# Performance work log

Measured on AMD Instinct MI355X. Metric: run time of the kernel, lower is better.

## Reference

```python
import jax, jax.numpy as jnp
import numpy as np

# BoxCoder weights and clamp from the torch module
WX, WY, WW, WH = 10.0, 10.0, 5.0, 5.0
BBOX_CLIP = float(np.log(1000.0 / 16.0))
SCORE_THRESH = 0.05
NMS_THRESH = 0.5
DET_PER_IMG = 100
MIN_SIZE = 0.01
B, N, C = 4, 4096, 91
IMG_H, IMG_W = 800, 1216


def setup_inputs() -> dict:
    key = jax.random.key(0)
    k1, k2, k3, k4, k5, k6 = jax.random.split(key, 6)
    class_logits = jax.random.normal(k1, (B * N, C), dtype=jnp.float32) * 2.0
    box_regression = jax.random.normal(k2, (B * N, C * 4), dtype=jnp.float32) * 0.5
    # valid xyxy proposals inside the image
    x1 = jax.random.uniform(k3, (B, N)) * (0.7 * IMG_W)
    y1 = jax.random.uniform(k4, (B, N)) * (0.7 * IMG_H)
    bw = jax.random.uniform(k5, (B, N)) * (0.25 * IMG_W) + 4.0
    bh = jax.random.uniform(k6, (B, N)) * (0.25 * IMG_H) + 4.0
    proposals = jnp.stack([x1, y1, x1 + bw, y1 + bh], axis=-1)
    image_shapes = jnp.tile(jnp.array([[IMG_H, IMG_W]], dtype=jnp.int32), (B, 1))
    return {"class_logits": class_logits, "box_regression": box_regression,
            "proposals": proposals, "image_shapes": image_shapes}


def decode_boxes(deltas, proposals):
    # deltas [N, C, 4], proposals [N, 4] xyxy -> pred boxes [N, C, 4]
    w = proposals[:, 2] - proposals[:, 0]
    h = proposals[:, 3] - proposals[:, 1]
    cx = proposals[:, 0] + 0.5 * w
    cy = proposals[:, 1] + 0.5 * h
    dx = deltas[..., 0] / WX
    dy = deltas[..., 1] / WY
    dw = jnp.minimum(deltas[..., 2] / WW, BBOX_CLIP)
    dh = jnp.minimum(deltas[..., 3] / WH, BBOX_CLIP)
    pcx = dx * w[:, None] + cx[:, None]
    pcy = dy * h[:, None] + cy[:, None]
    pw = jnp.exp(dw) * w[:, None]
    ph = jnp.exp(dh) * h[:, None]
    return jnp.stack([pcx - 0.5 * pw, pcy - 0.5 * ph,
                      pcx + 0.5 * pw, pcy + 0.5 * ph], axis=-1)


def iou_one_many(box, boxes):
    # box [4] vs boxes [M, 4]
    lt = jnp.maximum(box[:2], boxes[:, :2])
    rb = jnp.minimum(box[2:], boxes[:, 2:])
    wh = jnp.clip(rb - lt, 0.0)
    inter = wh[:, 0] * wh[:, 1]
    a1 = (box[2] - box[0]) * (box[3] - box[1])
    a2 = (boxes[:, 2] - boxes[:, 0]) * (boxes[:, 3] - boxes[:, 1])
    return inter / (a1 + a2 - inter)


def nms_keep(off_boxes, live):
    # greedy NMS on class-offset boxes; selection is non-differentiable
    off_boxes = jax.lax.stop_gradient(off_boxes)
    live = jax.lax.stop_gradient(live)

    def body(lv, _):
        i = jnp.argmax(lv)
        s = lv[i]
        iou = iou_one_many(off_boxes[i], off_boxes)
        lv = jnp.where(iou > NMS_THRESH, -jnp.inf, lv)
        lv = lv.at[i].set(-jnp.inf)
        return lv, (i, jnp.isfinite(s))

    _, (keep, kvalid) = jax.lax.scan(body, live, None, length=DET_PER_IMG)
    return keep, kvalid  # [DET_PER_IMG] each


def postprocess_one(logits, deltas, proposals, hw):
    # logits [N, C], deltas [N, C*4], proposals [N, 4], hw [2] float (H, W)
    num_classes = logits.shape[-1]
    boxes = decode_boxes(deltas.reshape(-1, num_classes, 4), proposals)  # [N, C, 4]
    Hh, Ww = hw[0], hw[1]
    boxes = jnp.stack([jnp.clip(boxes[..., 0], 0.0, Ww),
                       jnp.clip(boxes[..., 1], 0.0, Hh),
                       jnp.clip(boxes[..., 2], 0.0, Ww),
                       jnp.clip(boxes[..., 3], 0.0, Hh)], axis=-1)
    scores = jax.nn.softmax(logits, axis=-1)
    labels = jnp.broadcast_to(jnp.arange(num_classes, dtype=jnp.int32), scores.shape)
    # drop background class 0, flatten per-class candidates -> M = N*(C-1)
    boxes = boxes[:, 1:].reshape(-1, 4)
    scores = scores[:, 1:].reshape(-1)
    labels = labels[:, 1:].reshape(-1)
    ws = boxes[:, 2] - boxes[:, 0]
    hs = boxes[:, 3] - boxes[:, 1]
    valid = (scores > SCORE_THRESH) & (ws >= MIN_SIZE) & (hs >= MIN_SIZE)
    # batched_nms: per-class coordinate offset so classes never overlap
    max_coord = jnp.max(boxes)
    off_boxes = boxes + (labels.astype(boxes.dtype) * (max_coord + 1.0))[:, None]
    live = jnp.where(valid, scores, -jnp.inf)
    keep, kvalid = nms_keep(off_boxes, live)
    out_boxes = jnp.where(kvalid[:, None], boxes[keep], 0.0)
    out_scores = jnp.where(kvalid, scores[keep], 0.0)
    out_labels = jnp.where(kvalid, labels[keep], -1)
    return out_boxes, out_scores, out_labels


def reference(class_logits, box_regression, proposals, image_shapes):
    b, n, _ = proposals.shape
    num_classes = class_logits.shape[-1]
    logits = class_logits.reshape(b, n, num_classes)
    deltas = box_regression.reshape(b, n, num_classes * 4)
    hw = image_shapes.astype(logits.dtype)
    boxes, scores, labels = jax.vmap(postprocess_one)(logits, deltas, proposals, hw)
    return boxes, scores, labels
```

## Files before the change

kernel.cpp:

```cpp
#include <hip/hip_runtime.h>
#include <math.h>
#include <float.h>
#include <limits.h>

#define NBATCH 4
#define NPROP  4096
#define NCLS   91
#define NFG    90
#define NDET   100
#define CCAP   1024
#define BN     (NBATCH * NPROP)
#define SLOTS  (NFG * NDET)
#define FCAP   16384
#define CHUNK  128

static __device__ __forceinline__ float clampf(float x, float lo, float hi) {
    return fminf(fmaxf(x, lo), hi);
}

static __device__ __forceinline__ void decode_box(int b, int np, int c,
    const float* __restrict__ props, const float* __restrict__ deltas,
    float W, float H, float& bx1, float& by1, float& bx2, float& by2)
{
    const float* pr = props + ((size_t)b * NPROP + np) * 4;
    const float x1 = pr[0], y1 = pr[1], x2 = pr[2], y2 = pr[3];
    const float w = x2 - x1, h = y2 - y1;
    const float cx = x1 + 0.5f * w, cy = y1 + 0.5f * h;
    const float* d = deltas + (((size_t)b * NPROP + np) * NCLS + c) * 4;
    const float BBC = 4.135166556742356f;
    const float dx = d[0] / 10.0f;
    const float dy = d[1] / 10.0f;
    const float dw = fminf(d[2] / 5.0f, BBC);
    const float dh = fminf(d[3] / 5.0f, BBC);
    const float pcx = dx * w + cx;
    const float pcy = dy * h + cy;
    const float pw = expf(dw) * w;
    const float ph = expf(dh) * h;
    bx1 = clampf(pcx - 0.5f * pw, 0.0f, W);
    by1 = clampf(pcy - 0.5f * ph, 0.0f, H);
    bx2 = clampf(pcx + 0.5f * pw, 0.0f, W);
    by2 = clampf(pcy + 0.5f * ph, 0.0f, H);
}

static __device__ __forceinline__ bool iou_gt(const float4 S, const float4 Q, float aq)
{
    const float iw = fmaxf(fminf(S.z, Q.z) - fmaxf(S.x, Q.x), 0.0f);
    const float ih = fmaxf(fminf(S.w, Q.w) - fmaxf(S.y, Q.y), 0.0f);
    const float inter = iw * ih;
    const float as = (S.z - S.x) * (S.w - S.y);
    return inter / (as + aq - inter) > 0.5f;
}

static __device__ __forceinline__ int block_excl_scan(int v, int t, int* wtot)
{
    const int lane = t & 63, wid = t >> 6;
    int inc = v;
    #pragma unroll
    for (int s = 1; s < 64; s <<= 1) {
        const int u = __shfl_up(inc, s);
        if (lane >= s) inc += u;
    }
    if (lane == 63) wtot[wid] = inc;
    __syncthreads();
    int base = 0;
    for (int w2 = 0; w2 < wid; ++w2) base += wtot[w2];
    __syncthreads();
    return base + inc - v;
}

__global__ __launch_bounds__(256) void stats_mask_kernel(
    const float* __restrict__ logits, const float* __restrict__ props,
    const float* __restrict__ deltas, const int* __restrict__ imgsh,
    float2* __restrict__ stats, unsigned* __restrict__ mask)
{
    const int wavei = threadIdx.x >> 6;
    const int lane  = threadIdx.x & 63;
    const int p = blockIdx.x * 4 + wavei;
    const int b = p >> 12;
    const int np = p & (NPROP - 1);
    const float* lrow = logits + (size_t)p * NCLS;

    const float a  = lrow[lane];
    const float a2 = (lane + 64 < NCLS) ? lrow[lane + 64] : -INFINITY;

    float m = fmaxf(a, a2);
    #pragma unroll
    for (int s = 32; s > 0; s >>= 1) m = fmaxf(m, __shfl_down(m, s));
    m = __shfl(m, 0);

    const float e0 = expf(a - m);
    const float e1 = (lane + 64 < NCLS) ? expf(a2 - m) : 0.0f;
    float sum = e0 + e1;
    #pragma unroll
    for (int s = 32; s > 0; s >>= 1) sum += __shfl_down(sum, s);
    sum = __shfl(sum, 0);

    const float W = (float)imgsh[b * 2 + 1];
    const float H = (float)imgsh[b * 2 + 0];

    bool pass0 = ((e0 / sum) > 0.05f) && (lane >= 1);
    if (pass0) {
        float bx1, by1, bx2, by2;
        decode_box(b, np, lane, props, deltas, W, H, bx1, by1, bx2, by2);
        pass0 = ((bx2 - bx1) >= 0.01f) && ((by2 - by1) >= 0.01f);
    }
    bool pass1 = ((e1 / sum) > 0.05f);
    if (pass1) {
        float bx1, by1, bx2, by2;
        decode_box(b, np, lane + 64, props, deltas, W, H, bx1, by1, bx2, by2);
        pass1 = ((bx2 - bx1) >= 0.01f) && ((by2 - by1) >= 0.01f);
    }

    const unsigned long long b0 = __ballot(pass0);
    const unsigned long long b1 = __ballot(pass1);

    if (lane == 0) {
        stats[p] = make_float2(m, sum);
        mask[p]          = (unsigned)b0;
        mask[BN + p]     = (unsigned)(b0 >> 32);
        mask[2 * BN + p] = (unsigned)b1;
    }
}

__global__ __launch_bounds__(256) void class_nms_kernel(
    const float* __restrict__ logits, const float2* __restrict__ stats,
    const unsigned* __restrict__ mask,
    const float* __restrict__ props, const float* __restrict__ deltas,
    const int* __restrict__ imgsh, unsigned long long* __restrict__ svKeys)
{
    const int blk  = blockIdx.x;
    const int b    = blk / NFG;
    const int cm1  = blk % NFG;
    const int c    = cm1 + 1;
    const int t    = threadIdx.x;
    const int lane = t & 63;
    const int wid  = t >> 6;

    __shared__ unsigned long long sk[CCAP];
    __shared__ unsigned long long sks[CCAP];
    __shared__ float4 sbox[CCAP];
    __shared__ unsigned long long mrow[CHUNK][2];
    __shared__ float4 sOwn[NDET];
    __shared__ unsigned long long sPreW[2];
    __shared__ int wtot[4];
    __shared__ int s_ns;

    const float W = (float)imgsh[b * 2 + 1];
    const float H = (float)imgsh[b * 2 + 0];

    const unsigned* mp = mask + (size_t)(c >> 5) * BN + b * NPROP;
    const unsigned bit = 1u << (c & 31);

    int cnt = 0;
    #pragma unroll 4
    for (int np = t; np < NPROP; np += 256) cnt += (mp[np] & bit) ? 1 : 0;

    int v = cnt;
    #pragma unroll
    for (int s = 1; s < 64; s <<= 1) {
        const int u = __shfl_up(v, s);
        if (lane >= s) v += u;
    }
    if (lane == 63) wtot[wid] = v;
    __syncthreads();
    int base = 0;
    for (int w2 = 0; w2 < wid; ++w2) base += wtot[w2];
    int pos = base + v - cnt;
    const int ntot = wtot[0] + wtot[1] + wtot[2] + wtot[3];
    const int n = min(ntot, CCAP);
    if (n == 0) {
        for (int i = t; i < NDET; i += 256) svKeys[(size_t)blk * NDET + i] = 0ULL;
        return;
    }

    for (int np = t; np < NPROP; np += 256) {
        if (!(mp[np] & bit)) continue;
        const int p = b * NPROP + np;
        const float lg = logits[(size_t)p * NCLS + c];
        const float2 st = stats[p];
        const float score = expf(lg - st.x) / st.y;
        const unsigned flat = (unsigned)(np * NFG + cm1);
        const unsigned long long key =
            ((unsigned long long)__float_as_uint(score) << 32) | (unsigned)(~flat);
        if (pos < CCAP) sk[pos] = key;
        ++pos;
    }
    __syncthreads();

    {
        unsigned long long myk[4];
        int rnk[4] = {0, 0, 0, 0};
        #pragma unroll
        for (int e = 0; e < 4; ++e)
            myk[e] = (t + e * 256 < n) ? sk[t + e * 256] : 0ULL;
        #pragma unroll 4
        for (int j = 0; j < n; ++j) {
            const unsigned long long kj = sk[j];
            #pragma unroll
            for (int e = 0; e < 4; ++e) rnk[e] += (kj > myk[e]) ? 1 : 0;
        }
        #pragma unroll
        for (int e = 0; e < 4; ++e)
            if (t + e * 256 < n) sks[rnk[e]] = myk[e];
    }
    __syncthreads();

    for (int i = t; i < n; i += 256) {
        const unsigned flat = ~(unsigned)sks[i];
        const int np = flat / NFG;
        float bx1, by1, bx2, by2;
        decode_box(b, np, c, props, deltas, W, H, bx1, by1, bx2, by2);
        sbox[i] = make_float4(bx1, by1, bx2, by2);
    }
    if (t == 0) s_ns = 0;
    __syncthreads();

    int nsTot = 0;
    for (int cb = 0; cb < n && nsTot < NDET; cb += CHUNK) {
        const int C = min(CHUNK, n - cb);

        bool pre = false;
        if (t < C) {
            const float4 Q = sbox[cb + t];
            const float aq = (Q.z - Q.x) * (Q.w - Q.y);
            for (int l = 0; l < nsTot; ++l) {
                if (iou_gt(sOwn[l], Q, aq)) { pre = true; break; }
            }
        }
        const unsigned long long bal = __ballot(pre);
        if (t == 0)  sPreW[0] = bal;
        if (t == 64) sPreW[1] = bal;

        {
            const int r = t >> 1, w = t & 1;
            unsigned long long word = 0ULL;
            if (r < C) {
                const float4 R = sbox[cb + r];
                const int j0 = w * 64;
                const int jend = min(j0 + 64, C);
                for (int j = (j0 > r + 1 ? j0 : r + 1); j < jend; ++j) {
                    const float4 Q = sbox[cb + j];
                    const float aq = (Q.z - Q.x) * (Q.w - Q.y);
                    if (iou_gt(R, Q, aq)) word |= (1ULL << (j - j0));
                }
            }
            mrow[r][w] = word;
        }
        __syncthreads();

        if (t == 0) {
            unsigned long long S0 = sPreW[0], S1 = sPreW[1];
            int ns = nsTot;
            unsigned long long r0 = mrow[0][0], r1 = mrow[0][1];
            for (int i = 0; i < C && ns < NDET; ++i) {
                const unsigned long long nr0 = (i + 1 < C) ? mrow[i + 1][0] : 0ULL;
                const unsigned long long nr1 = (i + 1 < C) ? mrow[i + 1][1] : 0ULL;
                const bool dead = (i < 64) ? ((S0 >> i) & 1ULL)
                                           : ((S1 >> (i - 64)) & 1ULL);
                if (!dead) {
                    sOwn[ns] = sbox[cb + i];
                    svKeys[(size_t)blk * NDET + ns] = sks[cb + i];
                    ++ns;
                    S0 |= r0; S1 |= r1;
                }
                r0 = nr0; r1 = nr1;
            }
            s_ns = ns;
        }
        __syncthreads();
        nsTot = s_ns;
    }

    for (int i = nsTot + t; i < NDET; i += 256) svKeys[(size_t)blk * NDET + i] = 0ULL;
}

__global__ __launch_bounds__(1024) void select_kernel(
    const unsigned long long* __restrict__ svKeys,
    const float* __restrict__ props, const float* __restrict__ deltas,
    const int* __restrict__ imgsh, float* __restrict__ out)
{
    const int b = blockIdx.x;
    const int t = threadIdx.x;
    __shared__ unsigned long long F[FCAP];
    __shared__ int hist[4096];
    __shared__ int wtot[16];
    __shared__ int s_T, s_above, s_total;

    if (t == 0) { s_T = -1; s_above = 0; s_total = 0; }
    #pragma unroll
    for (int j = 0; j < 4; ++j) hist[t + j * 1024] = 0;

    const unsigned long long* src = svKeys + (size_t)b * SLOTS;
    unsigned long long keys[9];
    #pragma unroll
    for (int j = 0; j < 9; ++j) {
        const int s = t + j * 1024;
        keys[j] = (s < SLOTS) ? src[s] : 0ULL;
    }
    __syncthreads();

    #pragma unroll
    for (int j = 0; j < 9; ++j) {
        if (keys[j] != 0ULL) atomicAdd(&hist[(unsigned)(keys[j] >> 52)], 1);
    }
    __syncthreads();

    {
        const int gbase = (1023 - t) * 4;
        const int s0 = hist[gbase] + hist[gbase + 1] + hist[gbase + 2] + hist[gbase + 3];
        const int pre = block_excl_scan(s0, t, wtot);
        int acc = pre;
        for (int d = gbase + 3; d >= gbase; --d) {
            const int h = hist[d];
            if (acc < NDET && acc + h >= NDET) { s_T = d; s_above = acc; }
            acc += h;
        }
        if (t == 1023) s_total = acc;
    }
    __syncthreads();

    const int T = s_T;
    const int total = s_total;
    const int n2 = (T < 0) ? total : (s_above + hist[T]);
    const bool fast = (n2 <= 2048);

    int mycnt = 0;
    #pragma unroll
    for (int j = 0; j < 9; ++j) {
        const unsigned long long k = keys[j];
        const bool m = (k != 0ULL) && (fast ? (T < 0 || (int)(k >> 52) >= T) : true);
        mycnt += m ? 1 : 0;
    }
    int off = block_excl_scan(mycnt, t, wtot);
    #pragma unroll
    for (int j = 0; j < 9; ++j) {
        const unsigned long long k = keys[j];
        const bool m = (k != 0ULL) && (fast ? (T < 0 || (int)(k >> 52) >= T) : true);
        if (m) F[off++] = k;
    }
    const int nsort = fast ? n2 : total;

    int P = 128; while (P < nsort) P <<= 1;
    for (int i = nsort + t; i < P; i += 1024) F[i] = 0ULL;

    for (unsigned kk = 2; kk <= (unsigned)P; kk <<= 1) {
        for (unsigned jj = kk >> 1; jj > 0; jj >>= 1) {
            __syncthreads();
            for (unsigned i = t; i < (unsigned)P; i += 1024) {
                const unsigned ixj = i ^ jj;
                if (ixj > i) {
                    const unsigned long long x = F[i], y = F[ixj];
                    const bool up = ((i & kk) == 0);
                    if (up ? (x < y) : (x > y)) { F[i] = y; F[ixj] = x; }
                }
            }
        }
    }
    __syncthreads();

    float* oB = out + (size_t)b * NDET * 4;
    float* oS = out + (size_t)NBATCH * NDET * 4 + (size_t)b * NDET;
    float* oL = out + (size_t)NBATCH * NDET * 5 + (size_t)b * NDET;
    if (t < NDET) {
        const unsigned long long key = F[t];
        if (key != 0ULL) {
            const unsigned flat = ~(unsigned)key;
            const float score = __uint_as_float((unsigned)(key >> 32));
            const int np = flat / NFG;
            const int c  = (int)(flat - (unsigned)np * NFG) + 1;
            const float W = (float)imgsh[b * 2 + 1];
            const float H = (float)imgsh[b * 2 + 0];
            float bx1, by1, bx2, by2;
            decode_box(b, np, c, props, deltas, W, H, bx1, by1, bx2, by2);
            oB[t * 4 + 0] = bx1; oB[t * 4 + 1] = by1;
            oB[t * 4 + 2] = bx2; oB[t * 4 + 3] = by2;
            oS[t] = score;
            oL[t] = (float)c;
        } else {
            oB[t * 4 + 0] = 0.0f; oB[t * 4 + 1] = 0.0f;
            oB[t * 4 + 2] = 0.0f; oB[t * 4 + 3] = 0.0f;
            oS[t] = 0.0f; oL[t] = -1.0f;
        }
    }
}

extern "C" void kernel_launch(void* const* d_in, const int* in_sizes, int n_in,
                              void* d_out, int out_size, void* d_ws, size_t ws_size,
                              hipStream_t stream)
{
    const float* logits = (const float*)d_in[0];
    const float* deltas = (const float*)d_in[1];
    const float* props  = (const float*)d_in[2];
    const int*   imgsh  = (const int*)d_in[3];
    float* out = (float*)d_out;

    char* w = (char*)d_ws;
    float2* stats = (float2*)w;            w += (size_t)BN * sizeof(float2);
    unsigned* mask = (unsigned*)w;         w += (size_t)3 * BN * sizeof(unsigned);
    unsigned long long* svKeys = (unsigned long long*)w;
    w += (size_t)NBATCH * SLOTS * sizeof(unsigned long long);

    stats_mask_kernel<<<BN / 4, 256, 0, stream>>>(logits, props, deltas, imgsh, stats, mask);
    class_nms_kernel<<<NBATCH * NFG, 256, 0, stream>>>(
        logits, stats, mask, props, deltas, imgsh, svKeys);
    select_kernel<<<NBATCH, 1024, 0, stream>>>(svKeys, props, deltas, imgsh, out);
}
```

Before: 80.95 us.

## Precompute per-class CSR candidate key lists before class NMS

```diff
diff --git a/kernel.cpp b/kernel.cpp
--- a/kernel.cpp
+++ b/kernel.cpp
@@ -13,6 +13,7 @@
 #define SLOTS  (NFG * NDET)
 #define FCAP   16384
 #define CHUNK  128
+#define CSRCAP (NPROP * 19)
 
 static __device__ __forceinline__ float clampf(float x, float lo, float hi) {
     return fminf(fmaxf(x, lo), hi);
@@ -122,9 +123,76 @@
     }
 }
 
-__global__ __launch_bounds__(256) void class_nms_kernel(
+__global__ __launch_bounds__(1024) void csr_kernel(
     const float* __restrict__ logits, const float2* __restrict__ stats,
     const unsigned* __restrict__ mask,
+    int* __restrict__ clsCnt, int* __restrict__ clsOff,
+    unsigned long long* __restrict__ cKeys)
+{
+    const int b = blockIdx.x;
+    const int t = threadIdx.x;
+    __shared__ int hcnt[NFG];
+    __shared__ int hoff[NFG];
+    __shared__ int hfill[NFG];
+    __shared__ int scanbuf[128];
+
+    if (t < NFG) { hcnt[t] = 0; hfill[t] = 0; }
+    __syncthreads();
+
+    for (int np = t; np < NPROP; np += 1024) {
+        const int p = b * NPROP + np;
+        unsigned m0 = mask[p];
+        unsigned m1 = mask[BN + p];
+        unsigned m2 = mask[2 * BN + p];
+        while (m0) { const int c = __ffs(m0) - 1; m0 &= m0 - 1; atomicAdd(&hcnt[c - 1], 1); }
+        while (m1) { const int c = __ffs(m1) - 1 + 32; m1 &= m1 - 1; atomicAdd(&hcnt[c - 1], 1); }
+        while (m2) { const int c = __ffs(m2) - 1 + 64; m2 &= m2 - 1; atomicAdd(&hcnt[c - 1], 1); }
+    }
+    __syncthreads();
+
+    if (t < 128) scanbuf[t] = (t < NFG) ? hcnt[t] : 0;
+    __syncthreads();
+    for (int s = 1; s < 128; s <<= 1) {
+        int v = 0;
+        if (t < 128 && t >= s) v = scanbuf[t - s];
+        __syncthreads();
+        if (t < 128) scanbuf[t] += v;
+        __syncthreads();
+    }
+    if (t < NFG) {
+        hoff[t] = scanbuf[t] - hcnt[t];
+        clsCnt[b * NFG + t] = hcnt[t];
+        clsOff[b * NFG + t] = hoff[t];
+    }
+    __syncthreads();
+
+    unsigned long long* dst = cKeys + (size_t)b * CSRCAP;
+    for (int np = t; np < NPROP; np += 1024) {
+        const int p = b * NPROP + np;
+        unsigned m0 = mask[p];
+        unsigned m1 = mask[BN + p];
+        unsigned m2 = mask[2 * BN + p];
+        if (!(m0 | m1 | m2)) continue;
+        const float2 st = stats[p];
+        const float* lrow = logits + (size_t)p * NCLS;
+        #define EMIT(c_) { \
+            const int cm1_ = (c_) - 1; \
+            const float score_ = expf(lrow[(c_)] - st.x) / st.y; \
+            const unsigned flat_ = (unsigned)(np * NFG + cm1_); \
+            const unsigned long long key_ = \
+                ((unsigned long long)__float_as_uint(score_) << 32) | (unsigned)(~flat_); \
+            const int pos_ = atomicAdd(&hfill[cm1_], 1); \
+            dst[hoff[cm1_] + pos_] = key_; }
+        while (m0) { const int c = __ffs(m0) - 1; m0 &= m0 - 1; EMIT(c); }
+        while (m1) { const int c = __ffs(m1) - 1 + 32; m1 &= m1 - 1; EMIT(c); }
+        while (m2) { const int c = __ffs(m2) - 1 + 64; m2 &= m2 - 1; EMIT(c); }
+        #undef EMIT
+    }
+}
+
+__global__ __launch_bounds__(256) void class_nms_kernel(
+    const int* __restrict__ clsCnt, const int* __restrict__ clsOff,
+    const unsigned long long* __restrict__ cKeys,
     const float* __restrict__ props, const float* __restrict__ deltas,
     const int* __restrict__ imgsh, unsigned long long* __restrict__ svKeys)
 {
@@ -133,8 +201,6 @@
     const int cm1  = blk % NFG;
     const int c    = cm1 + 1;
     const int t    = threadIdx.x;
-    const int lane = t & 63;
-    const int wid  = t >> 6;
 
     __shared__ unsigned long long sk[CCAP];
     __shared__ unsigned long long sks[CCAP];
@@ -142,49 +208,15 @@
     __shared__ unsigned long long mrow[CHUNK][2];
     __shared__ float4 sOwn[NDET];
     __shared__ unsigned long long sPreW[2];
-    __shared__ int wtot[4];
     __shared__ int s_ns;
 
-    const float W = (float)imgsh[b * 2 + 1];
-    const float H = (float)imgsh[b * 2 + 0];
-
-    const unsigned* mp = mask + (size_t)(c >> 5) * BN + b * NPROP;
-    const unsigned bit = 1u << (c & 31);
-
-    int cnt = 0;
-    #pragma unroll 4
-    for (int np = t; np < NPROP; np += 256) cnt += (mp[np] & bit) ? 1 : 0;
-
-    int v = cnt;
-    #pragma unroll
-    for (int s = 1; s < 64; s <<= 1) {
-        const int u = __shfl_up(v, s);
-        if (lane >= s) v += u;
-    }
-    if (lane == 63) wtot[wid] = v;
-    __syncthreads();
-    int base = 0;
-    for (int w2 = 0; w2 < wid; ++w2) base += wtot[w2];
-    int pos = base + v - cnt;
-    const int ntot = wtot[0] + wtot[1] + wtot[2] + wtot[3];
-    const int n = min(ntot, CCAP);
+    const int n = min(clsCnt[blk], CCAP);
     if (n == 0) {
         for (int i = t; i < NDET; i += 256) svKeys[(size_t)blk * NDET + i] = 0ULL;
         return;
     }
-
-    for (int np = t; np < NPROP; np += 256) {
-        if (!(mp[np] & bit)) continue;
-        const int p = b * NPROP + np;
-        const float lg = logits[(size_t)p * NCLS + c];
-        const float2 st = stats[p];
-        const float score = expf(lg - st.x) / st.y;
-        const unsigned flat = (unsigned)(np * NFG + cm1);
-        const unsigned long long key =
-            ((unsigned long long)__float_as_uint(score) << 32) | (unsigned)(~flat);
-        if (pos < CCAP) sk[pos] = key;
-        ++pos;
-    }
+    const unsigned long long* src = cKeys + (size_t)b * CSRCAP + clsOff[blk];
+    for (int i = t; i < n; i += 256) sk[i] = src[i];
     __syncthreads();
 
     {
@@ -205,6 +237,8 @@
     }
     __syncthreads();
 
+    const float W = (float)imgsh[b * 2 + 1];
+    const float H = (float)imgsh[b * 2 + 0];
     for (int i = t; i < n; i += 256) {
         const unsigned flat = ~(unsigned)sks[i];
         const int np = flat / NFG;
@@ -399,9 +433,14 @@
     unsigned* mask = (unsigned*)w;         w += (size_t)3 * BN * sizeof(unsigned);
     unsigned long long* svKeys = (unsigned long long*)w;
     w += (size_t)NBATCH * SLOTS * sizeof(unsigned long long);
+    int* clsCnt = (int*)w;                 w += 4096;
+    int* clsOff = (int*)w;                 w += 4096;
+    unsigned long long* cKeys = (unsigned long long*)w;
+    w += (size_t)NBATCH * CSRCAP * sizeof(unsigned long long);
 
     stats_mask_kernel<<<BN / 4, 256, 0, stream>>>(logits, props, deltas, imgsh, stats, mask);
+    csr_kernel<<<NBATCH, 1024, 0, stream>>>(logits, stats, mask, clsCnt, clsOff, cKeys);
     class_nms_kernel<<<NBATCH * NFG, 256, 0, stream>>>(
-        logits, stats, mask, props, deltas, imgsh, svKeys);
+        clsCnt, clsOff, cKeys, props, deltas, imgsh, svKeys);
     select_kernel<<<NBATCH, 1024, 0, stream>>>(svKeys, props, deltas, imgsh, out);
 }
```

Result: slower. 110.4 us (+36.4%).

## Transpose per-proposal class masks into per-class bitsets for candidate compaction

Applied to the files above, without the earlier changes.

```diff
diff --git a/kernel.cpp b/kernel.cpp
--- a/kernel.cpp
+++ b/kernel.cpp
@@ -13,6 +13,7 @@
 #define SLOTS  (NFG * NDET)
 #define FCAP   16384
 #define CHUNK  128
+#define NWORD  128
 
 static __device__ __forceinline__ float clampf(float x, float lo, float hi) {
     return fminf(fmaxf(x, lo), hi);
@@ -122,9 +123,35 @@
     }
 }
 
+__global__ __launch_bounds__(256) void maskt_kernel(
+    const unsigned* __restrict__ mask, unsigned* __restrict__ maskT)
+{
+    const int blk = blockIdx.x;
+    const int b = blk >> 4;
+    const int s = blk & 15;
+    const int t = threadIdx.x;
+    __shared__ unsigned lm[3 * 256];
+
+    #pragma unroll
+    for (int j = 0; j < 3; ++j)
+        lm[j * 256 + t] = mask[(size_t)j * BN + b * NPROP + s * 256 + t];
+    __syncthreads();
+
+    for (int idx = t; idx < NCLS * 8; idx += 256) {
+        const int c = idx >> 3, w = idx & 7;
+        const int plane = c >> 5, bitpos = c & 31;
+        const unsigned* src = &lm[plane * 256 + w * 32];
+        unsigned word = 0;
+        #pragma unroll
+        for (int k = 0; k < 32; ++k)
+            word |= ((src[k] >> bitpos) & 1u) << k;
+        maskT[((size_t)(b * NCLS + c)) * NWORD + s * 8 + w] = word;
+    }
+}
+
 __global__ __launch_bounds__(256) void class_nms_kernel(
     const float* __restrict__ logits, const float2* __restrict__ stats,
-    const unsigned* __restrict__ mask,
+    const unsigned* __restrict__ maskT,
     const float* __restrict__ props, const float* __restrict__ deltas,
     const int* __restrict__ imgsh, unsigned long long* __restrict__ svKeys)
 {
@@ -134,56 +161,54 @@
     const int c    = cm1 + 1;
     const int t    = threadIdx.x;
     const int lane = t & 63;
-    const int wid  = t >> 6;
-
+
+    __shared__ unsigned wbuf[NWORD];
+    __shared__ int wt2[2];
     __shared__ unsigned long long sk[CCAP];
     __shared__ unsigned long long sks[CCAP];
     __shared__ float4 sbox[CCAP];
     __shared__ unsigned long long mrow[CHUNK][2];
     __shared__ float4 sOwn[NDET];
     __shared__ unsigned long long sPreW[2];
-    __shared__ int wtot[4];
     __shared__ int s_ns;
 
-    const float W = (float)imgsh[b * 2 + 1];
-    const float H = (float)imgsh[b * 2 + 0];
-
-    const unsigned* mp = mask + (size_t)(c >> 5) * BN + b * NPROP;
-    const unsigned bit = 1u << (c & 31);
-
-    int cnt = 0;
-    #pragma unroll 4
-    for (int np = t; np < NPROP; np += 256) cnt += (mp[np] & bit) ? 1 : 0;
-
-    int v = cnt;
+    const unsigned* col = maskT + ((size_t)(b * NCLS + c)) * NWORD;
+    if (t < NWORD) wbuf[t] = col[t];
+    __syncthreads();
+
+    const int pc = (t < NWORD) ? __popc(wbuf[t]) : 0;
+    int inc = pc;
     #pragma unroll
     for (int s = 1; s < 64; s <<= 1) {
-        const int u = __shfl_up(v, s);
-        if (lane >= s) v += u;
-    }
-    if (lane == 63) wtot[wid] = v;
-    __syncthreads();
-    int base = 0;
-    for (int w2 = 0; w2 < wid; ++w2) base += wtot[w2];
-    int pos = base + v - cnt;
-    const int ntot = wtot[0] + wtot[1] + wtot[2] + wtot[3];
+        const int u = __shfl_up(inc, s);
+        if (lane >= s) inc += u;
+    }
+    if (lane == 63 && (t >> 6) < 2) wt2[t >> 6] = inc;
+    __syncthreads();
+    const int ntot = wt2[0] + wt2[1];
     const int n = min(ntot, CCAP);
     if (n == 0) {
         for (int i = t; i < NDET; i += 256) svKeys[(size_t)blk * NDET + i] = 0ULL;
         return;
     }
-
-    for (int np = t; np < NPROP; np += 256) {
-        if (!(mp[np] & bit)) continue;
-        const int p = b * NPROP + np;
-        const float lg = logits[(size_t)p * NCLS + c];
-        const float2 st = stats[p];
-        const float score = expf(lg - st.x) / st.y;
-        const unsigned flat = (unsigned)(np * NFG + cm1);
-        const unsigned long long key =
-            ((unsigned long long)__float_as_uint(score) << 32) | (unsigned)(~flat);
-        if (pos < CCAP) sk[pos] = key;
-        ++pos;
+    const int myoff = ((t >> 6) == 1 ? wt2[0] : 0) + inc - pc;
+
+    if (t < NWORD) {
+        unsigned wv = wbuf[t];
+        int o = myoff;
+        while (wv) {
+            const int k = __ffs(wv) - 1; wv &= wv - 1;
+            const int np = t * 32 + k;
+            const int p = b * NPROP + np;
+            const float lg = logits[(size_t)p * NCLS + c];
+            const float2 st = stats[p];
+            const float score = expf(lg - st.x) / st.y;
+            const unsigned flat = (unsigned)(np * NFG + cm1);
+            const unsigned long long key =
+                ((unsigned long long)__float_as_uint(score) << 32) | (unsigned)(~flat);
+            if (o < CCAP) sk[o] = key;
+            ++o;
+        }
     }
     __syncthreads();
 
@@ -205,6 +230,8 @@
     }
     __syncthreads();
 
+    const float W = (float)imgsh[b * 2 + 1];
+    const float H = (float)imgsh[b * 2 + 0];
     for (int i = t; i < n; i += 256) {
         const unsigned flat = ~(unsigned)sks[i];
         const int np = flat / NFG;
@@ -399,9 +426,12 @@
     unsigned* mask = (unsigned*)w;         w += (size_t)3 * BN * sizeof(unsigned);
     unsigned long long* svKeys = (unsigned long long*)w;
     w += (size_t)NBATCH * SLOTS * sizeof(unsigned long long);
+    unsigned* maskT = (unsigned*)w;
+    w += (size_t)NBATCH * NCLS * NWORD * sizeof(unsigned);
 
     stats_mask_kernel<<<BN / 4, 256, 0, stream>>>(logits, props, deltas, imgsh, stats, mask);
+    maskt_kernel<<<NBATCH * 16, 256, 0, stream>>>(mask, maskT);
     class_nms_kernel<<<NBATCH * NFG, 256, 0, stream>>>(
-        logits, stats, mask, props, deltas, imgsh, svKeys);
+        logits, stats, maskT, props, deltas, imgsh, svKeys);
     select_kernel<<<NBATCH, 1024, 0, stream>>>(svKeys, props, deltas, imgsh, out);
 }
```

After: 74.73 us (median of 2 runs). 1.08x faster.

## Scatter candidates into per-class buckets via atomics in the decode kernel

Applied to the files above, without the earlier changes.

```diff
diff --git a/kernel.cpp b/kernel.cpp
--- a/kernel.cpp
+++ b/kernel.cpp
@@ -13,6 +13,7 @@
 #define SLOTS  (NFG * NDET)
 #define FCAP   16384
 #define CHUNK  128
+#define CPAD   32
 
 static __device__ __forceinline__ float clampf(float x, float lo, float hi) {
     return fminf(fmaxf(x, lo), hi);
@@ -68,10 +69,11 @@
     return base + inc - v;
 }
 
-__global__ __launch_bounds__(256) void stats_mask_kernel(
+__global__ __launch_bounds__(256) void fused_decode_kernel(
     const float* __restrict__ logits, const float* __restrict__ props,
     const float* __restrict__ deltas, const int* __restrict__ imgsh,
-    float2* __restrict__ stats, unsigned* __restrict__ mask)
+    int* __restrict__ cntPad, unsigned long long* __restrict__ cKeys,
+    float4* __restrict__ cBox)
 {
     const int wavei = threadIdx.x >> 6;
     const int lane  = threadIdx.x & 63;
@@ -98,101 +100,64 @@
     const float W = (float)imgsh[b * 2 + 1];
     const float H = (float)imgsh[b * 2 + 0];
 
-    bool pass0 = ((e0 / sum) > 0.05f) && (lane >= 1);
-    if (pass0) {
+    #pragma unroll
+    for (int half = 0; half < 2; ++half) {
+        const int c = lane + half * 64;
+        if (c < 1 || c >= NCLS) continue;
+        const float e = half ? e1 : e0;
+        const float score = e / sum;
+        if (!(score > 0.05f)) continue;
         float bx1, by1, bx2, by2;
-        decode_box(b, np, lane, props, deltas, W, H, bx1, by1, bx2, by2);
-        pass0 = ((bx2 - bx1) >= 0.01f) && ((by2 - by1) >= 0.01f);
-    }
-    bool pass1 = ((e1 / sum) > 0.05f);
-    if (pass1) {
-        float bx1, by1, bx2, by2;
-        decode_box(b, np, lane + 64, props, deltas, W, H, bx1, by1, bx2, by2);
-        pass1 = ((bx2 - bx1) >= 0.01f) && ((by2 - by1) >= 0.01f);
-    }
-
-    const unsigned long long b0 = __ballot(pass0);
-    const unsigned long long b1 = __ballot(pass1);
-
-    if (lane == 0) {
-        stats[p] = make_float2(m, sum);
-        mask[p]          = (unsigned)b0;
-        mask[BN + p]     = (unsigned)(b0 >> 32);
-        mask[2 * BN + p] = (unsigned)b1;
+        decode_box(b, np, c, props, deltas, W, H, bx1, by1, bx2, by2);
+        if (!((bx2 - bx1) >= 0.01f && (by2 - by1) >= 0.01f)) continue;
+        const int cm1 = c - 1;
+        const unsigned flat = (unsigned)(np * NFG + cm1);
+        const unsigned long long key =
+            ((unsigned long long)__float_as_uint(score) << 32) | (unsigned)(~flat);
+        const int bucket = b * NFG + cm1;
+        const int pos = atomicAdd(&cntPad[bucket * CPAD], 1);
+        if (pos < CCAP) {
+            cKeys[(size_t)bucket * CCAP + pos] = key;
+            cBox[(size_t)bucket * CCAP + pos]  = make_float4(bx1, by1, bx2, by2);
+        }
     }
 }
 
 __global__ __launch_bounds__(256) void class_nms_kernel(
-    const float* __restrict__ logits, const float2* __restrict__ stats,
-    const unsigned* __restrict__ mask,
-    const float* __restrict__ props, const float* __restrict__ deltas,
-    const int* __restrict__ imgsh, unsigned long long* __restrict__ svKeys)
+    const int* __restrict__ cntPad, const unsigned long long* __restrict__ cKeys,
+    const float4* __restrict__ cBox, unsigned long long* __restrict__ svKeys)
 {
     const int blk  = blockIdx.x;
-    const int b    = blk / NFG;
-    const int cm1  = blk % NFG;
-    const int c    = cm1 + 1;
     const int t    = threadIdx.x;
-    const int lane = t & 63;
-    const int wid  = t >> 6;
 
     __shared__ unsigned long long sk[CCAP];
     __shared__ unsigned long long sks[CCAP];
-    __shared__ float4 sbox[CCAP];
+    __shared__ float4 sboxS[CCAP];
     __shared__ unsigned long long mrow[CHUNK][2];
     __shared__ float4 sOwn[NDET];
     __shared__ unsigned long long sPreW[2];
-    __shared__ int wtot[4];
     __shared__ int s_ns;
 
-    const float W = (float)imgsh[b * 2 + 1];
-    const float H = (float)imgsh[b * 2 + 0];
-
-    const unsigned* mp = mask + (size_t)(c >> 5) * BN + b * NPROP;
-    const unsigned bit = 1u << (c & 31);
-
-    int cnt = 0;
-    #pragma unroll 4
-    for (int np = t; np < NPROP; np += 256) cnt += (mp[np] & bit) ? 1 : 0;
-
-    int v = cnt;
-    #pragma unroll
-    for (int s = 1; s < 64; s <<= 1) {
-        const int u = __shfl_up(v, s);
-        if (lane >= s) v += u;
-    }
-    if (lane == 63) wtot[wid] = v;
-    __syncthreads();
-    int base = 0;
-    for (int w2 = 0; w2 < wid; ++w2) base += wtot[w2];
-    int pos = base + v - cnt;
-    const int ntot = wtot[0] + wtot[1] + wtot[2] + wtot[3];
-    const int n = min(ntot, CCAP);
+    const int n = min(cntPad[blk * CPAD], CCAP);
     if (n == 0) {
         for (int i = t; i < NDET; i += 256) svKeys[(size_t)blk * NDET + i] = 0ULL;
         return;
     }
-
-    for (int np = t; np < NPROP; np += 256) {
-        if (!(mp[np] & bit)) continue;
-        const int p = b * NPROP + np;
-        const float lg = logits[(size_t)p * NCLS + c];
-        const float2 st = stats[p];
-        const float score = expf(lg - st.x) / st.y;
-        const unsigned flat = (unsigned)(np * NFG + cm1);
-        const unsigned long long key =
-            ((unsigned long long)__float_as_uint(score) << 32) | (unsigned)(~flat);
-        if (pos < CCAP) sk[pos] = key;
-        ++pos;
-    }
+    const unsigned long long* srcK = cKeys + (size_t)blk * CCAP;
+    const float4* srcB = cBox + (size_t)blk * CCAP;
+    for (int i = t; i < n; i += 256) sk[i] = srcK[i];
     __syncthreads();
 
     {
         unsigned long long myk[4];
+        float4 myb[4];
         int rnk[4] = {0, 0, 0, 0};
         #pragma unroll
-        for (int e = 0; e < 4; ++e)
-            myk[e] = (t + e * 256 < n) ? sk[t + e * 256] : 0ULL;
+        for (int e = 0; e < 4; ++e) {
+            const int i = t + e * 256;
+            myk[e] = (i < n) ? sk[i] : 0ULL;
+            myb[e] = (i < n) ? srcB[i] : make_float4(0.f, 0.f, 0.f, 0.f);
+        }
         #pragma unroll 4
         for (int j = 0; j < n; ++j) {
             const unsigned long long kj = sk[j];
@@ -200,17 +165,9 @@
             for (int e = 0; e < 4; ++e) rnk[e] += (kj > myk[e]) ? 1 : 0;
         }
         #pragma unroll
-        for (int e = 0; e < 4; ++e)
-            if (t + e * 256 < n) sks[rnk[e]] = myk[e];
-    }
-    __syncthreads();
-
-    for (int i = t; i < n; i += 256) {
-        const unsigned flat = ~(unsigned)sks[i];
-        const int np = flat / NFG;
-        float bx1, by1, bx2, by2;
-        decode_box(b, np, c, props, deltas, W, H, bx1, by1, bx2, by2);
-        sbox[i] = make_float4(bx1, by1, bx2, by2);
+        for (int e = 0; e < 4; ++e) {
+            if (t + e * 256 < n) { sks[rnk[e]] = myk[e]; sboxS[rnk[e]] = myb[e]; }
+        }
     }
     if (t == 0) s_ns = 0;
     __syncthreads();
@@ -221,7 +178,7 @@
 
         bool pre = false;
         if (t < C) {
-            const float4 Q = sbox[cb + t];
+            const float4 Q = sboxS[cb + t];
             const float aq = (Q.z - Q.x) * (Q.w - Q.y);
             for (int l = 0; l < nsTot; ++l) {
                 if (iou_gt(sOwn[l], Q, aq)) { pre = true; break; }
@@ -235,11 +192,11 @@
             const int r = t >> 1, w = t & 1;
             unsigned long long word = 0ULL;
             if (r < C) {
-                const float4 R = sbox[cb + r];
+                const float4 R = sboxS[cb + r];
                 const int j0 = w * 64;
                 const int jend = min(j0 + 64, C);
                 for (int j = (j0 > r + 1 ? j0 : r + 1); j < jend; ++j) {
-                    const float4 Q = sbox[cb + j];
+                    const float4 Q = sboxS[cb + j];
                     const float aq = (Q.z - Q.x) * (Q.w - Q.y);
                     if (iou_gt(R, Q, aq)) word |= (1ULL << (j - j0));
                 }
@@ -258,7 +215,7 @@
                 const bool dead = (i < 64) ? ((S0 >> i) & 1ULL)
                                            : ((S1 >> (i - 64)) & 1ULL);
                 if (!dead) {
-                    sOwn[ns] = sbox[cb + i];
+                    sOwn[ns] = sboxS[cb + i];
                     svKeys[(size_t)blk * NDET + ns] = sks[cb + i];
                     ++ns;
                     S0 |= r0; S1 |= r1;
@@ -395,13 +352,17 @@
     float* out = (float*)d_out;
 
     char* w = (char*)d_ws;
-    float2* stats = (float2*)w;            w += (size_t)BN * sizeof(float2);
-    unsigned* mask = (unsigned*)w;         w += (size_t)3 * BN * sizeof(unsigned);
+    int* cntPad = (int*)w;                 w += (size_t)NBATCH * NFG * CPAD * sizeof(int);
     unsigned long long* svKeys = (unsigned long long*)w;
     w += (size_t)NBATCH * SLOTS * sizeof(unsigned long long);
-
-    stats_mask_kernel<<<BN / 4, 256, 0, stream>>>(logits, props, deltas, imgsh, stats, mask);
-    class_nms_kernel<<<NBATCH * NFG, 256, 0, stream>>>(
-        logits, stats, mask, props, deltas, imgsh, svKeys);
+    unsigned long long* cKeys = (unsigned long long*)w;
+    w += (size_t)NBATCH * NFG * CCAP * sizeof(unsigned long long);
+    float4* cBox = (float4*)w;
+    w += (size_t)NBATCH * NFG * CCAP * sizeof(float4);
+
+    hipMemsetAsync(cntPad, 0, (size_t)NBATCH * NFG * CPAD * sizeof(int), stream);
+    fused_decode_kernel<<<BN / 4, 256, 0, stream>>>(
+        logits, props, deltas, imgsh, cntPad, cKeys, cBox);
+    class_nms_kernel<<<NBATCH * NFG, 256, 0, stream>>>(cntPad, cKeys, cBox, svKeys);
     select_kernel<<<NBATCH, 1024, 0, stream>>>(svKeys, props, deltas, imgsh, out);
 }
```

Measured after the change: 76.22 us. 1.06x faster.
